# Performance work log

Hardware: AMD Instinct MI355X
Metric: run time of the kernel (lower is better)

## Reference

```python
import jax, jax.numpy as jnp
import numpy as np

B, S, D = 2, 2048, 1024
H, HD = 16, 64


def setup_inputs() -> dict:
    key = jax.random.key(0)
    ks = jax.random.split(key, 6)
    hidden_states = jax.random.normal(ks[0], (B, S, D), dtype=jnp.float32)
    c_attn_w = jax.random.normal(ks[1], (D, 3 * D), dtype=jnp.float32) * 0.02
    c_attn_b = jnp.zeros((3 * D,), dtype=jnp.float32)
    c_proj_w = jax.random.normal(ks[2], (D, D), dtype=jnp.float32) * 0.02
    c_proj_b = jnp.zeros((D,), dtype=jnp.float32)
    basis = jax.random.normal(ks[3], (H, HD, HD), dtype=jnp.float32) * 0.1
    projectors = jnp.einsum('hdr,her->hde', basis, basis)  # basis @ basis.T per head
    return {
        'hidden_states': hidden_states,
        'c_attn_w': c_attn_w,
        'c_attn_b': c_attn_b,
        'c_proj_w': c_proj_w,
        'c_proj_b': c_proj_b,
        'projectors': projectors,
    }


def reference(hidden_states, c_attn_w, c_attn_b, c_proj_w, c_proj_b, projectors):
    # GPT2 Conv1D: out = x @ W + b
    qkv = hidden_states @ c_attn_w + c_attn_b  # [B,S,3D]
    q, k, v = jnp.split(qkv, 3, axis=-1)
    # split heads -> [B,H,S,HD]
    def split_heads(t):
        return t.reshape(B, S, H, HD).transpose(0, 2, 1, 3)
    q, k, v = split_heads(q), split_heads(k), split_heads(v)
    scores = jnp.einsum('bhqd,bhkd->bhqk', q, k) / jnp.sqrt(jnp.float32(HD))
    causal = jnp.tril(jnp.ones((S, S), dtype=bool))
    scores = jnp.where(causal, scores, jnp.finfo(scores.dtype).min)
    probs = jax.nn.softmax(scores, axis=-1)
    attn = jnp.einsum('bhqk,bhkd->bhqd', probs, v)  # [B,H,S,HD]
    # per-head basis projector applied to attention output
    attn = jnp.einsum('bhsd,hde->bhse', attn, projectors)
    # merge heads -> [B,S,D]
    attn = attn.transpose(0, 2, 1, 3).reshape(B, S, D)
    out = attn @ c_proj_w + c_proj_b
    return out
```

## Files before the change

kernel.cpp:

```cpp
#include <hip/hip_runtime.h>
#include <hip/hip_bf16.h>

typedef __attribute__((ext_vector_type(8))) short bhalf8;
typedef __attribute__((ext_vector_type(4))) float f32x4;
typedef __attribute__((ext_vector_type(8))) unsigned short u16x8;
typedef __attribute__((ext_vector_type(4))) unsigned short u16x4;

#define BDIM 2
#define SDIM 2048
#define DDIM 1024
#define HDIM 16
#define HDHD 64
#define EXPB 12.0f

#define GLD16(gaddr, laddr)                                                          \
  __builtin_amdgcn_global_load_lds(                                                  \
      (const __attribute__((address_space(1))) unsigned int*)(gaddr),                \
      (__attribute__((address_space(3))) unsigned int*)(laddr), 16, 0, 0)

__device__ __forceinline__ unsigned short f2bf(float f) {
  unsigned u = __builtin_bit_cast(unsigned, f);
  u += 0x7fffu + ((u >> 16) & 1u);
  return (unsigned short)(u >> 16);
}
__device__ __forceinline__ unsigned short f2bfc(float f) {
  return __builtin_bit_cast(unsigned short, __float2bfloat16(f));
}
__device__ __forceinline__ float bf2f(unsigned short u) {
  return __builtin_bit_cast(float, (unsigned)u << 16);
}

__global__ __launch_bounds__(256) void cvt_hidden(const float* __restrict__ x,
                                                  unsigned short* __restrict__ y) {
  size_t i = ((size_t)blockIdx.x * 256 + threadIdx.x) * 4;
  f32x4 v = *(const f32x4*)(x + i);
  u16x4 o;
  o[0] = f2bf(v[0]); o[1] = f2bf(v[1]); o[2] = f2bf(v[2]); o[3] = f2bf(v[3]);
  *(u16x4*)(y + i) = o;
}

__global__ __launch_bounds__(256) void transpose_cvt(const float* __restrict__ W,
                                                     unsigned short* __restrict__ Wt,
                                                     int R, int C) {
  __shared__ float tl[32][33];
  int rt = blockIdx.x * 32, ct = blockIdx.y * 32;
  int r8 = threadIdx.x >> 5, c = threadIdx.x & 31;
#pragma unroll
  for (int i = 0; i < 4; i++)
    tl[r8 + i * 8][c] = W[(size_t)(rt + r8 + i * 8) * C + ct + c];
  __syncthreads();
#pragma unroll
  for (int i = 0; i < 4; i++)
    Wt[(size_t)(ct + r8 + i * 8) * R + rt + c] = f2bf(tl[c][r8 + i * 8]);
}

__global__ __launch_bounds__(256) void make_wproj(const float* __restrict__ proj,
                                                  const float* __restrict__ wproj,
                                                  unsigned short* __restrict__ WT) {
  int h = blockIdx.x, ot = blockIdx.y * 64;
  __shared__ float Pl[64][65];
  __shared__ float Wl[64][65];
  int t = threadIdx.x;
#pragma unroll
  for (int i = 0; i < 16; i++) {
    int idx = t + 256 * i;
    int a = idx >> 6, bc = idx & 63;
    Pl[a][bc] = proj[(size_t)h * 4096 + idx];
    Wl[a][bc] = wproj[(size_t)(h * 64 + a) * 1024 + ot + bc];
  }
  __syncthreads();
  int d = t & 63, ob = t >> 6;
#pragma unroll
  for (int i = 0; i < 16; i++) {
    int o = ob + i * 4;
    float acc = 0.f;
#pragma unroll
    for (int e = 0; e < 64; e++) acc += Pl[d][e] * Wl[e][o];
    WT[(size_t)(ot + o) * 1024 + h * 64 + d] = f2bf(acc);
  }
}

__global__ __launch_bounds__(256) void gemm_qkv(
    const unsigned short* __restrict__ A, const unsigned short* __restrict__ Bt,
    const float* __restrict__ bias,
    unsigned short* __restrict__ q, unsigned short* __restrict__ k,
    unsigned short* __restrict__ v, int M, int N, int K) {
  __shared__ unsigned short As[128 * 64];
  __shared__ unsigned short Bs[128 * 64];
  const int tid = threadIdx.x;
  const int orig = blockIdx.y * 24 + blockIdx.x;
  const int swz = (orig & 7) * 96 + (orig >> 3);
  const int m0 = (swz / 24) * 128, n0 = (swz % 24) * 128;
  f32x4 acc[4][4];
#pragma unroll
  for (int m = 0; m < 4; m++)
#pragma unroll
    for (int n = 0; n < 4; n++) acc[m][n] = f32x4{0.f, 0.f, 0.f, 0.f};
  const int w = tid >> 6, lane = tid & 63;
  const int wr = (w >> 1) * 64, wc = (w & 1) * 64;
  const int lrow = lane & 15, lg = lane >> 4;

  for (int kt = 0; kt < K; kt += 64) {
    __syncthreads();
#pragma unroll
    for (int i = 0; i < 4; i++) {
      int cl = tid + 256 * i;
      int r = cl >> 3, c = cl & 7;
      int sc = (c ^ (r & 7)) * 8;
      GLD16(A + (size_t)(m0 + r) * K + kt + sc, &As[cl * 8]);
      GLD16(Bt + (size_t)(n0 + r) * K + kt + sc, &Bs[cl * 8]);
    }
    __syncthreads();
#pragma unroll
    for (int kk = 0; kk < 2; kk++) {
      bhalf8 af[4], bfr[4];
#pragma unroll
      for (int m = 0; m < 4; m++) {
        int r = wr + m * 16 + lrow;
        int ch = r * 8 + ((kk * 4 + lg) ^ (r & 7));
        af[m] = *(const bhalf8*)(&As[ch * 8]);
      }
#pragma unroll
      for (int n = 0; n < 4; n++) {
        int r = wc + n * 16 + lrow;
        int ch = r * 8 + ((kk * 4 + lg) ^ (r & 7));
        bfr[n] = *(const bhalf8*)(&Bs[ch * 8]);
      }
#pragma unroll
      for (int m = 0; m < 4; m++)
#pragma unroll
        for (int n = 0; n < 4; n++)
          acc[m][n] = __builtin_amdgcn_mfma_f32_16x16x32_bf16(af[m], bfr[n], acc[m][n], 0, 0, 0);
    }
  }
  const int g = lane >> 4, il = lane & 15;
#pragma unroll
  for (int m = 0; m < 4; m++) {
    int rowb = wr + m * 16 + 4 * g;
#pragma unroll
    for (int n = 0; n < 4; n++) {
      int col = n0 + wc + n * 16 + il;
      float bs = bias[col];
#pragma unroll
      for (int r = 0; r < 4; r++) {
        int row = m0 + rowb + r;
        float val = acc[m][n][r] + bs;
        int which = col >> 10, hh = (col >> 6) & 15, hd = col & 63;
        int b = row >> 11, s = row & 2047;
        size_t idx = ((size_t)(b * 16 + hh) * SDIM + s) * HDHD + hd;
        unsigned short bv = f2bf(which == 0 ? val * 0.1803368801f : val);
        if (which == 0) q[idx] = bv;
        else if (which == 1) k[idx] = bv;
        else v[idx] = bv;
      }
    }
  }
}

__global__ __launch_bounds__(128) void gemm_out(
    const unsigned short* __restrict__ A, const unsigned short* __restrict__ Bt,
    const float* __restrict__ bias, float* __restrict__ Cf, int M, int N, int K) {
  __shared__ unsigned short As[64][72];
  __shared__ unsigned short Bs[128][72];
  const int tid = threadIdx.x;
  const int orig = blockIdx.y * 8 + blockIdx.x;
  const int swz = (orig & 7) * 64 + (orig >> 3);
  const int m0 = (swz / 8) * 64, n0 = (swz % 8) * 128;
  f32x4 acc[4][4];
#pragma unroll
  for (int m = 0; m < 4; m++)
#pragma unroll
    for (int n = 0; n < 4; n++) acc[m][n] = f32x4{0.f, 0.f, 0.f, 0.f};
  const int w = tid >> 6, lane = tid & 63;
  const int wc = w * 64;
  const int lrow = lane & 15, lk = (lane >> 4) * 8;

  for (int kt = 0; kt < K; kt += 64) {
    __syncthreads();
#pragma unroll
    for (int i = 0; i < 4; i++) {
      int cch = tid + 128 * i;
      int r = cch >> 3, c8 = cch & 7;
      *(u16x8*)(&As[r][c8 * 8]) = *(const u16x8*)(A + (size_t)(m0 + r) * K + kt + c8 * 8);
    }
#pragma unroll
    for (int i = 0; i < 8; i++) {
      int cch = tid + 128 * i;
      int r = cch >> 3, c8 = cch & 7;
      *(u16x8*)(&Bs[r][c8 * 8]) = *(const u16x8*)(Bt + (size_t)(n0 + r) * K + kt + c8 * 8);
    }
    __syncthreads();
#pragma unroll
    for (int kk = 0; kk < 2; kk++) {
      bhalf8 af[4], bfr[4];
#pragma unroll
      for (int m = 0; m < 4; m++) af[m] = *(const bhalf8*)(&As[m * 16 + lrow][kk * 32 + lk]);
#pragma unroll
      for (int n = 0; n < 4; n++) bfr[n] = *(const bhalf8*)(&Bs[wc + n * 16 + lrow][kk * 32 + lk]);
#pragma unroll
      for (int m = 0; m < 4; m++)
#pragma unroll
        for (int n = 0; n < 4; n++)
          acc[m][n] = __builtin_amdgcn_mfma_f32_16x16x32_bf16(af[m], bfr[n], acc[m][n], 0, 0, 0);
    }
  }
  const int g = lane >> 4, il = lane & 15;
#pragma unroll
  for (int m = 0; m < 4; m++) {
    int rowb = m * 16 + 4 * g;
#pragma unroll
    for (int n = 0; n < 4; n++) {
      int col = n0 + wc + n * 16 + il;
      float bs = bias[col];
#pragma unroll
      for (int r = 0; r < 4; r++)
        Cf[(size_t)(m0 + rowb + r) * N + col] = acc[m][n][r] + bs;
    }
  }
}

__global__ __launch_bounds__(128, 3) void attn_partial(const unsigned short* __restrict__ Q,
                                                       const unsigned short* __restrict__ Kb,
                                                       const unsigned short* __restrict__ Vb,
                                                       unsigned short* __restrict__ PO,
                                                       float2* __restrict__ ML) {
  __shared__ unsigned short Ks[64][72];
  __shared__ unsigned short Vt[64][72];
  __shared__ unsigned short Ps[2][32][72];
  const int bh = blockIdx.x;
  const int qt = 31 - blockIdx.y;
  const int seg = blockIdx.z;
  const int a = qt >> 3, bq = qt & 7;
  const int nseg = a + 1;
  if (seg >= nseg) return;
  const int k0 = seg * 8;
  const int k1 = min(k0 + 8, qt + 1);

  const int tid = threadIdx.x;
  const int w = tid >> 6, lane = tid & 63;
  const int g = lane >> 4, il = lane & 15;
  const int qbase = qt * 64 + w * 32;
  const size_t bhS = (size_t)bh * SDIM;

  bhalf8 qf[2][2];
#pragma unroll
  for (int f = 0; f < 2; f++) {
    const unsigned short* qp = Q + (bhS + qbase + f * 16 + il) * HDHD + g * 8;
    qf[f][0] = *(const bhalf8*)(qp);
    qf[f][1] = *(const bhalf8*)(qp + 32);
  }
  f32x4 oacc[2][4];
#pragma unroll
  for (int f = 0; f < 2; f++)
#pragma unroll
    for (int i = 0; i < 4; i++) oacc[f][i] = f32x4{0.f, 0.f, 0.f, 0.f};
  float lrun[2] = {0.f, 0.f};

  const int krow = tid >> 1;
  const int kchk = (tid & 1) * 32;
  const int vd0 = (tid & 31) * 2;
  const int vkg = (tid >> 5) * 16;

  u16x8 kr[4];
  unsigned vr[16];
  {
    const size_t kb0 = (bhS + (size_t)k0 * 64) * HDHD;
    const unsigned short* ksrc = Kb + kb0 + krow * HDHD + kchk;
#pragma unroll
    for (int i = 0; i < 4; i++) kr[i] = *(const u16x8*)(ksrc + i * 8);
    const unsigned short* vsrc = Vb + kb0 + (size_t)vkg * HDHD + vd0;
#pragma unroll
    for (int i = 0; i < 16; i++) vr[i] = *(const unsigned*)(vsrc + i * HDHD);
  }

  for (int kt = k0; kt < k1; kt++) {
    __syncthreads();
#pragma unroll
    for (int i = 0; i < 4; i++) *(u16x8*)(&Ks[krow][kchk + i * 8]) = kr[i];
    {
      u16x8 lo0, lo1, hi0, hi1;
#pragma unroll
      for (int i = 0; i < 8; i++) {
        lo0[i] = (unsigned short)(vr[i] & 0xffffu); hi0[i] = (unsigned short)(vr[i] >> 16);
      }
#pragma unroll
      for (int i = 0; i < 8; i++) {
        lo1[i] = (unsigned short)(vr[8 + i] & 0xffffu); hi1[i] = (unsigned short)(vr[8 + i] >> 16);
      }
      *(u16x8*)(&Vt[vd0][vkg]) = lo0;     *(u16x8*)(&Vt[vd0][vkg + 8]) = lo1;
      *(u16x8*)(&Vt[vd0 + 1][vkg]) = hi0; *(u16x8*)(&Vt[vd0 + 1][vkg + 8]) = hi1;
    }
    if (kt + 1 < k1) {
      const size_t kbn = (bhS + (size_t)(kt + 1) * 64) * HDHD;
      const unsigned short* ksrc = Kb + kbn + krow * HDHD + kchk;
#pragma unroll
      for (int i = 0; i < 4; i++) kr[i] = *(const u16x8*)(ksrc + i * 8);
      const unsigned short* vsrc = Vb + kbn + (size_t)vkg * HDHD + vd0;
#pragma unroll
      for (int i = 0; i < 16; i++) vr[i] = *(const unsigned*)(vsrc + i * HDHD);
    }
    __syncthreads();
    f32x4 s[2][4];
#pragma unroll
    for (int f = 0; f < 2; f++)
#pragma unroll
      for (int c = 0; c < 4; c++) s[f][c] = f32x4{0.f, 0.f, 0.f, 0.f};
#pragma unroll
    for (int c = 0; c < 4; c++) {
      bhalf8 kf0 = *(const bhalf8*)(&Ks[c * 16 + il][g * 8]);
      bhalf8 kf1 = *(const bhalf8*)(&Ks[c * 16 + il][32 + g * 8]);
#pragma unroll
      for (int f = 0; f < 2; f++) {
        s[f][c] = __builtin_amdgcn_mfma_f32_16x16x32_bf16(kf0, qf[f][0], s[f][c], 0, 0, 0);
        s[f][c] = __builtin_amdgcn_mfma_f32_16x16x32_bf16(kf1, qf[f][1], s[f][c], 0, 0, 0);
      }
    }
    const bool diag = (kt == qt);
#pragma unroll
    for (int f = 0; f < 2; f++) {
      const int thr = w * 32 + f * 16 + il;
      float rs = 0.f;
#pragma unroll
      for (int c = 0; c < 4; c++) {
        u16x4 pk;
#pragma unroll
        for (int r = 0; r < 4; r++) {
          float v = s[f][c][r];
          if (diag && (c * 16 + 4 * g + r > thr)) v = -1e30f;
          float pv = exp2f(v - EXPB);
          rs += pv;
          pk[r] = f2bfc(pv);
        }
        *(u16x4*)(&Ps[w][f * 16 + il][c * 16 + 4 * g]) = pk;
      }
      rs += __shfl_xor(rs, 16);
      rs += __shfl_xor(rs, 32);
      lrun[f] += rs;
    }
#pragma unroll
    for (int kk = 0; kk < 2; kk++) {
      bhalf8 pf0 = *(const bhalf8*)(&Ps[w][il][kk * 32 + g * 8]);
      bhalf8 pf1 = *(const bhalf8*)(&Ps[w][16 + il][kk * 32 + g * 8]);
#pragma unroll
      for (int df = 0; df < 4; df++) {
        bhalf8 vf = *(const bhalf8*)(&Vt[df * 16 + il][kk * 32 + g * 8]);
        oacc[0][df] = __builtin_amdgcn_mfma_f32_16x16x32_bf16(vf, pf0, oacc[0][df], 0, 0, 0);
        oacc[1][df] = __builtin_amdgcn_mfma_f32_16x16x32_bf16(vf, pf1, oacc[1][df], 0, 0, 0);
      }
    }
  }
  const int pidx = bh * 80 + 4 * a * (a + 1) + bq * (a + 1) + seg;
  __syncthreads();
#pragma unroll
  for (int f = 0; f < 2; f++) {
    float inv = 1.f / lrun[f];
#pragma unroll
    for (int df = 0; df < 4; df++) {
      u16x4 o;
#pragma unroll
      for (int r = 0; r < 4; r++) o[r] = f2bfc(oacc[f][df][r] * inv);
      *(u16x4*)(&Ks[w * 32 + f * 16 + il][df * 16 + 4 * g]) = o;
    }
  }
  if (g == 0) {
#pragma unroll
    for (int f = 0; f < 2; f++)
      ML[(size_t)pidx * 64 + w * 32 + f * 16 + il] = make_float2(EXPB, lrun[f]);
  }
  __syncthreads();
  {
    const int row = tid >> 1, half = (tid & 1) * 32;
    unsigned short* dst = PO + (size_t)pidx * 4096 + (size_t)row * 64 + half;
#pragma unroll
    for (int c8 = 0; c8 < 4; c8++)
      *(u16x8*)(dst + c8 * 8) = *(const u16x8*)(&Ks[row][half + c8 * 8]);
  }
}

__global__ __launch_bounds__(256) void attn_reduce(const unsigned short* __restrict__ PO,
                                                   const float2* __restrict__ ML,
                                                   unsigned short* __restrict__ Om) {
  const int bh = blockIdx.x, qt = blockIdx.y;
  const int a = qt >> 3, bq = qt & 7;
  const int nseg = a + 1;
  const int base = bh * 80 + 4 * a * (a + 1) + bq * (a + 1);
  const int t = threadIdx.x;
  const int r = t >> 2, dc = (t & 3) * 16;
  float2 mls[4];
  float M = -1e30f;
#pragma unroll
  for (int s = 0; s < 4; s++) {
    if (s < nseg) { mls[s] = ML[(size_t)(base + s) * 64 + r]; M = fmaxf(M, mls[s].x); }
  }
  float L = 0.f;
  float O[16];
#pragma unroll
  for (int j = 0; j < 16; j++) O[j] = 0.f;
#pragma unroll
  for (int s = 0; s < 4; s++) {
    if (s < nseg) {
      float wgt = mls[s].y * exp2f(mls[s].x - M);
      L += wgt;
      const unsigned short* p = PO + (size_t)(base + s) * 4096 + r * 64 + dc;
      u16x8 p0 = *(const u16x8*)p, p1 = *(const u16x8*)(p + 8);
#pragma unroll
      for (int j = 0; j < 8; j++) O[j] += wgt * bf2f(p0[j]);
#pragma unroll
      for (int j = 0; j < 8; j++) O[8 + j] += wgt * bf2f(p1[j]);
    }
  }
  float inv = 1.f / L;
  const int b = bh >> 4, h = bh & 15;
  size_t orow = ((size_t)b * SDIM + qt * 64 + r) * DDIM + h * HDHD + dc;
  u16x8 o0, o1;
#pragma unroll
  for (int j = 0; j < 8; j++) o0[j] = f2bfc(O[j] * inv);
#pragma unroll
  for (int j = 0; j < 8; j++) o1[j] = f2bfc(O[8 + j] * inv);
  *(u16x8*)(Om + orow) = o0;
  *(u16x8*)(Om + orow + 8) = o1;
}

__global__ __launch_bounds__(128, 2) void attn_direct(const unsigned short* __restrict__ Q,
                                                      const unsigned short* __restrict__ Kb,
                                                      const unsigned short* __restrict__ Vb,
                                                      unsigned short* __restrict__ Om) {
  __shared__ unsigned short Ks[64][72];
  __shared__ unsigned short Vt[64][72];
  __shared__ unsigned short Ps[2][32][72];
  const int bh = blockIdx.x;
  const int qt = 31 - blockIdx.y;
  const int tid = threadIdx.x;
  const int w = tid >> 6, lane = tid & 63;
  const int g = lane >> 4, il = lane & 15;
  const int qbase = qt * 64 + w * 32;
  const size_t bhS = (size_t)bh * SDIM;
  bhalf8 qf[2][2];
#pragma unroll
  for (int f = 0; f < 2; f++) {
    const unsigned short* qp = Q + (bhS + qbase + f * 16 + il) * HDHD + g * 8;
    qf[f][0] = *(const bhalf8*)(qp);
    qf[f][1] = *(const bhalf8*)(qp + 32);
  }
  f32x4 oacc[2][4];
#pragma unroll
  for (int f = 0; f < 2; f++)
#pragma unroll
    for (int i = 0; i < 4; i++) oacc[f][i] = f32x4{0.f, 0.f, 0.f, 0.f};
  float lrun[2] = {0.f, 0.f};
  const int krow = tid >> 1, kchk = (tid & 1) * 32;
  const int vd0 = (tid & 31) * 2, vkg = (tid >> 5) * 16;
  const int nt = qt + 1;
  for (int kt = 0; kt < nt; kt++) {
    const size_t kbase = (bhS + (size_t)kt * 64) * HDHD;
    __syncthreads();
    {
      const unsigned short* src = Kb + kbase + krow * HDHD + kchk;
#pragma unroll
      for (int i = 0; i < 4; i++) *(u16x8*)(&Ks[krow][kchk + i * 8]) = *(const u16x8*)(src + i * 8);
    }
    {
      const unsigned short* vsrc = Vb + kbase + (size_t)vkg * HDHD + vd0;
      u16x8 lo0, lo1, hi0, hi1;
#pragma unroll
      for (int i = 0; i < 8; i++) {
        unsigned vv = *(const unsigned*)(vsrc + i * HDHD);
        lo0[i] = (unsigned short)(vv & 0xffffu); hi0[i] = (unsigned short)(vv >> 16);
      }
#pragma unroll
      for (int i = 0; i < 8; i++) {
        unsigned vv = *(const unsigned*)(vsrc + (8 + i) * HDHD);
        lo1[i] = (unsigned short)(vv & 0xffffu); hi1[i] = (unsigned short)(vv >> 16);
      }
      *(u16x8*)(&Vt[vd0][vkg]) = lo0;     *(u16x8*)(&Vt[vd0][vkg + 8]) = lo1;
      *(u16x8*)(&Vt[vd0 + 1][vkg]) = hi0; *(u16x8*)(&Vt[vd0 + 1][vkg + 8]) = hi1;
    }
    __syncthreads();
    f32x4 s[2][4];
#pragma unroll
    for (int f = 0; f < 2; f++)
#pragma unroll
      for (int c = 0; c < 4; c++) s[f][c] = f32x4{0.f, 0.f, 0.f, 0.f};
#pragma unroll
    for (int c = 0; c < 4; c++) {
      bhalf8 kf0 = *(const bhalf8*)(&Ks[c * 16 + il][g * 8]);
      bhalf8 kf1 = *(const bhalf8*)(&Ks[c * 16 + il][32 + g * 8]);
#pragma unroll
      for (int f = 0; f < 2; f++) {
        s[f][c] = __builtin_amdgcn_mfma_f32_16x16x32_bf16(kf0, qf[f][0], s[f][c], 0, 0, 0);
        s[f][c] = __builtin_amdgcn_mfma_f32_16x16x32_bf16(kf1, qf[f][1], s[f][c], 0, 0, 0);
      }
    }
    const bool diag = (kt == qt);
#pragma unroll
    for (int f = 0; f < 2; f++) {
      const int thr = w * 32 + f * 16 + il;
      float rs = 0.f;
#pragma unroll
      for (int c = 0; c < 4; c++) {
        u16x4 pk;
#pragma unroll
        for (int r = 0; r < 4; r++) {
          float v = s[f][c][r];
          if (diag && (c * 16 + 4 * g + r > thr)) v = -1e30f;
          float pv = exp2f(v - EXPB);
          rs += pv;
          pk[r] = f2bfc(pv);
        }
        *(u16x4*)(&Ps[w][f * 16 + il][c * 16 + 4 * g]) = pk;
      }
      rs += __shfl_xor(rs, 16);
      rs += __shfl_xor(rs, 32);
      lrun[f] += rs;
    }
#pragma unroll
    for (int kk = 0; kk < 2; kk++) {
      bhalf8 pf0 = *(const bhalf8*)(&Ps[w][il][kk * 32 + g * 8]);
      bhalf8 pf1 = *(const bhalf8*)(&Ps[w][16 + il][kk * 32 + g * 8]);
#pragma unroll
      for (int df = 0; df < 4; df++) {
        bhalf8 vf = *(const bhalf8*)(&Vt[df * 16 + il][kk * 32 + g * 8]);
        oacc[0][df] = __builtin_amdgcn_mfma_f32_16x16x32_bf16(vf, pf0, oacc[0][df], 0, 0, 0);
        oacc[1][df] = __builtin_amdgcn_mfma_f32_16x16x32_bf16(vf, pf1, oacc[1][df], 0, 0, 0);
      }
    }
  }
  __syncthreads();
#pragma unroll
  for (int f = 0; f < 2; f++) {
    float inv = 1.f / lrun[f];
#pragma unroll
    for (int df = 0; df < 4; df++) {
      u16x4 o;
#pragma unroll
      for (int r = 0; r < 4; r++) o[r] = f2bfc(oacc[f][df][r] * inv);
      *(u16x4*)(&Ks[w * 32 + f * 16 + il][df * 16 + 4 * g]) = o;
    }
  }
  __syncthreads();
  {
    const int row = tid >> 1, half = (tid & 1) * 32;
    const int b = bh >> 4, h = bh & 15;
    size_t obase = ((size_t)b * SDIM + qt * 64 + row) * DDIM + h * HDHD + half;
#pragma unroll
    for (int c8 = 0; c8 < 4; c8++)
      *(u16x8*)(Om + obase + c8 * 8) = *(const u16x8*)(&Ks[row][half + c8 * 8]);
  }
}

extern "C" void kernel_launch(void* const* d_in, const int* in_sizes, int n_in,
                              void* d_out, int out_size, void* d_ws, size_t ws_size,
                              hipStream_t stream) {
  const float* hidden = (const float*)d_in[0];
  const float* attn_w = (const float*)d_in[1];
  const float* attn_b = (const float*)d_in[2];
  const float* proj_w = (const float*)d_in[3];
  const float* proj_b = (const float*)d_in[4];
  const float* projectors = (const float*)d_in[5];
  float* out = (float*)d_out;
  char* ws = (char*)d_ws;
  (void)in_sizes; (void)n_in; (void)out_size;

  unsigned short* hseq   = (unsigned short*)(ws);
  unsigned short* wqkvT  = (unsigned short*)(ws + 8388608);
  unsigned short* qb     = (unsigned short*)(ws + 14680064);
  unsigned short* kb     = (unsigned short*)(ws + 23068672);
  unsigned short* vb     = (unsigned short*)(ws + 31457280);
  unsigned short* attnM  = (unsigned short*)(ws + 39845888);
  unsigned short* wprojT = (unsigned short*)(ws + 48234496);
  unsigned short* PO     = (unsigned short*)(ws + 50331648);
  float2*         ML2    = (float2*)(ws + 71303168);
  const size_t ws_needed = 71303168 + 1310720;

  cvt_hidden<<<dim3(4096), dim3(256), 0, stream>>>(hidden, hseq);
  transpose_cvt<<<dim3(32, 96), dim3(256), 0, stream>>>(attn_w, wqkvT, 1024, 3072);
  make_wproj<<<dim3(16, 16), dim3(256), 0, stream>>>(projectors, proj_w, wprojT);
  gemm_qkv<<<dim3(24, 32), dim3(256), 0, stream>>>(hseq, wqkvT, attn_b,
                                                   qb, kb, vb, 4096, 3072, 1024);
  if (ws_size >= ws_needed) {
    attn_partial<<<dim3(32, 32, 4), dim3(128), 0, stream>>>(qb, kb, vb, PO, ML2);
    attn_reduce<<<dim3(32, 32), dim3(256), 0, stream>>>(PO, ML2, attnM);
  } else {
    attn_direct<<<dim3(32, 32), dim3(128), 0, stream>>>(qb, kb, vb, attnM);
  }
  gemm_out<<<dim3(8, 64), dim3(128), 0, stream>>>(attnM, wprojT, proj_b, out,
                                                  4096, 1024, 1024);
}
```

Measured before the change: 162.3 us.

## Process two key tiles per attention iteration and fuse preprocessing kernels

```diff
diff --git a/kernel.cpp b/kernel.cpp
--- a/kernel.cpp
+++ b/kernel.cpp
@@ -30,53 +30,56 @@
   return __builtin_bit_cast(float, (unsigned)u << 16);
 }
 
-__global__ __launch_bounds__(256) void cvt_hidden(const float* __restrict__ x,
-                                                  unsigned short* __restrict__ y) {
-  size_t i = ((size_t)blockIdx.x * 256 + threadIdx.x) * 4;
-  f32x4 v = *(const f32x4*)(x + i);
-  u16x4 o;
-  o[0] = f2bf(v[0]); o[1] = f2bf(v[1]); o[2] = f2bf(v[2]); o[3] = f2bf(v[3]);
-  *(u16x4*)(y + i) = o;
-}
-
-__global__ __launch_bounds__(256) void transpose_cvt(const float* __restrict__ W,
-                                                     unsigned short* __restrict__ Wt,
-                                                     int R, int C) {
-  __shared__ float tl[32][33];
-  int rt = blockIdx.x * 32, ct = blockIdx.y * 32;
-  int r8 = threadIdx.x >> 5, c = threadIdx.x & 31;
-#pragma unroll
-  for (int i = 0; i < 4; i++)
-    tl[r8 + i * 8][c] = W[(size_t)(rt + r8 + i * 8) * C + ct + c];
-  __syncthreads();
-#pragma unroll
-  for (int i = 0; i < 4; i++)
-    Wt[(size_t)(ct + r8 + i * 8) * R + rt + c] = f2bf(tl[c][r8 + i * 8]);
-}
-
-__global__ __launch_bounds__(256) void make_wproj(const float* __restrict__ proj,
+__global__ __launch_bounds__(256) void preprocess(const float* __restrict__ hidden,
+                                                  unsigned short* __restrict__ hseq,
+                                                  const float* __restrict__ attn_w,
+                                                  unsigned short* __restrict__ wqkvT,
+                                                  const float* __restrict__ proj,
                                                   const float* __restrict__ wproj,
-                                                  unsigned short* __restrict__ WT) {
-  int h = blockIdx.x, ot = blockIdx.y * 64;
-  __shared__ float Pl[64][65];
-  __shared__ float Wl[64][65];
-  int t = threadIdx.x;
-#pragma unroll
-  for (int i = 0; i < 16; i++) {
-    int idx = t + 256 * i;
-    int a = idx >> 6, bc = idx & 63;
-    Pl[a][bc] = proj[(size_t)h * 4096 + idx];
-    Wl[a][bc] = wproj[(size_t)(h * 64 + a) * 1024 + ot + bc];
-  }
-  __syncthreads();
-  int d = t & 63, ob = t >> 6;
-#pragma unroll
-  for (int i = 0; i < 16; i++) {
-    int o = ob + i * 4;
-    float acc = 0.f;
-#pragma unroll
-    for (int e = 0; e < 64; e++) acc += Pl[d][e] * Wl[e][o];
-    WT[(size_t)(ot + o) * 1024 + h * 64 + d] = f2bf(acc);
+                                                  unsigned short* __restrict__ wprojT) {
+  __shared__ float smem[2 * 64 * 65];
+  const int bid = blockIdx.x;
+  const int t = threadIdx.x;
+  if (bid < 4096) {
+    size_t i = ((size_t)bid * 256 + t) * 4;
+    f32x4 v = *(const f32x4*)(hidden + i);
+    u16x4 o;
+    o[0] = f2bf(v[0]); o[1] = f2bf(v[1]); o[2] = f2bf(v[2]); o[3] = f2bf(v[3]);
+    *(u16x4*)(hseq + i) = o;
+  } else if (bid < 7168) {
+    float (*tl)[33] = (float(*)[33])smem;
+    const int tt = bid - 4096;
+    const int rt = (tt & 31) * 32, ct = (tt >> 5) * 32;
+    const int r8 = t >> 5, c = t & 31;
+#pragma unroll
+    for (int i = 0; i < 4; i++)
+      tl[r8 + i * 8][c] = attn_w[(size_t)(rt + r8 + i * 8) * 3072 + ct + c];
+    __syncthreads();
+#pragma unroll
+    for (int i = 0; i < 4; i++)
+      wqkvT[(size_t)(ct + r8 + i * 8) * 1024 + rt + c] = f2bf(tl[c][r8 + i * 8]);
+  } else {
+    float (*Pl)[65] = (float(*)[65])smem;
+    float (*Wl)[65] = (float(*)[65])(smem + 64 * 65);
+    const int tt = bid - 7168;
+    const int h = tt & 15, ot = (tt >> 4) * 64;
+#pragma unroll
+    for (int i = 0; i < 16; i++) {
+      int idx = t + 256 * i;
+      int a = idx >> 6, bc = idx & 63;
+      Pl[a][bc] = proj[(size_t)h * 4096 + idx];
+      Wl[a][bc] = wproj[(size_t)(h * 64 + a) * 1024 + ot + bc];
+    }
+    __syncthreads();
+    int d = t & 63, ob = t >> 6;
+#pragma unroll
+    for (int i = 0; i < 16; i++) {
+      int o = ob + i * 4;
+      float acc = 0.f;
+#pragma unroll
+      for (int e = 0; e < 64; e++) acc += Pl[d][e] * Wl[e][o];
+      wprojT[(size_t)(ot + o) * 1024 + h * 64 + d] = f2bf(acc);
+    }
   }
 }
 
@@ -219,14 +222,14 @@
   }
 }
 
-__global__ __launch_bounds__(128, 3) void attn_partial(const unsigned short* __restrict__ Q,
+__global__ __launch_bounds__(128, 2) void attn_partial(const unsigned short* __restrict__ Q,
                                                        const unsigned short* __restrict__ Kb,
                                                        const unsigned short* __restrict__ Vb,
                                                        unsigned short* __restrict__ PO,
                                                        float2* __restrict__ ML) {
-  __shared__ unsigned short Ks[64][72];
-  __shared__ unsigned short Vt[64][72];
-  __shared__ unsigned short Ps[2][32][72];
+  __shared__ unsigned short Ks[128][72];
+  __shared__ unsigned short Vt[64][136];
+  __shared__ unsigned short Ps[2][32][136];
   const int bh = blockIdx.x;
   const int qt = 31 - blockIdx.y;
   const int seg = blockIdx.z;
@@ -256,89 +259,96 @@
     for (int i = 0; i < 4; i++) oacc[f][i] = f32x4{0.f, 0.f, 0.f, 0.f};
   float lrun[2] = {0.f, 0.f};
 
-  const int krow = tid >> 1;
-  const int kchk = (tid & 1) * 32;
   const int vd0 = (tid & 31) * 2;
   const int vkg = (tid >> 5) * 16;
 
-  u16x8 kr[4];
-  unsigned vr[16];
-  {
-    const size_t kb0 = (bhS + (size_t)k0 * 64) * HDHD;
-    const unsigned short* ksrc = Kb + kb0 + krow * HDHD + kchk;
-#pragma unroll
-    for (int i = 0; i < 4; i++) kr[i] = *(const u16x8*)(ksrc + i * 8);
-    const unsigned short* vsrc = Vb + kb0 + (size_t)vkg * HDHD + vd0;
-#pragma unroll
-    for (int i = 0; i < 16; i++) vr[i] = *(const unsigned*)(vsrc + i * HDHD);
-  }
-
-  for (int kt = k0; kt < k1; kt++) {
-    __syncthreads();
-#pragma unroll
-    for (int i = 0; i < 4; i++) *(u16x8*)(&Ks[krow][kchk + i * 8]) = kr[i];
-    {
+  u16x8 kr[8];
+  unsigned vr[32];
+#define LOADP(ktv)                                                                    \
+  {                                                                                   \
+    const unsigned short* ksrc = Kb + (bhS + (size_t)(ktv) * 64 + tid) * HDHD;        \
+    _Pragma("unroll")                                                                 \
+    for (int i = 0; i < 8; i++) kr[i] = *(const u16x8*)(ksrc + i * 8);                \
+    _Pragma("unroll")                                                                 \
+    for (int h = 0; h < 2; h++) {                                                     \
+      const unsigned short* vsrc =                                                    \
+          Vb + (bhS + (size_t)((ktv) + h) * 64 + vkg) * HDHD + vd0;                   \
+      _Pragma("unroll")                                                               \
+      for (int i = 0; i < 16; i++) vr[h * 16 + i] = *(const unsigned*)(vsrc + i * HDHD); \
+    }                                                                                 \
+  }
+
+  LOADP(k0);
+
+  for (int kt = k0; kt < k1; kt += 2) {
+    __syncthreads();
+#pragma unroll
+    for (int i = 0; i < 8; i++) *(u16x8*)(&Ks[tid][i * 8]) = kr[i];
+#pragma unroll
+    for (int h = 0; h < 2; h++) {
       u16x8 lo0, lo1, hi0, hi1;
 #pragma unroll
       for (int i = 0; i < 8; i++) {
-        lo0[i] = (unsigned short)(vr[i] & 0xffffu); hi0[i] = (unsigned short)(vr[i] >> 16);
+        unsigned vv = vr[h * 16 + i];
+        lo0[i] = (unsigned short)(vv & 0xffffu); hi0[i] = (unsigned short)(vv >> 16);
       }
 #pragma unroll
       for (int i = 0; i < 8; i++) {
-        lo1[i] = (unsigned short)(vr[8 + i] & 0xffffu); hi1[i] = (unsigned short)(vr[8 + i] >> 16);
-      }
-      *(u16x8*)(&Vt[vd0][vkg]) = lo0;     *(u16x8*)(&Vt[vd0][vkg + 8]) = lo1;
-      *(u16x8*)(&Vt[vd0 + 1][vkg]) = hi0; *(u16x8*)(&Vt[vd0 + 1][vkg + 8]) = hi1;
-    }
-    if (kt + 1 < k1) {
-      const size_t kbn = (bhS + (size_t)(kt + 1) * 64) * HDHD;
-      const unsigned short* ksrc = Kb + kbn + krow * HDHD + kchk;
-#pragma unroll
-      for (int i = 0; i < 4; i++) kr[i] = *(const u16x8*)(ksrc + i * 8);
-      const unsigned short* vsrc = Vb + kbn + (size_t)vkg * HDHD + vd0;
-#pragma unroll
-      for (int i = 0; i < 16; i++) vr[i] = *(const unsigned*)(vsrc + i * HDHD);
-    }
-    __syncthreads();
-    f32x4 s[2][4];
-#pragma unroll
-    for (int f = 0; f < 2; f++)
-#pragma unroll
-      for (int c = 0; c < 4; c++) s[f][c] = f32x4{0.f, 0.f, 0.f, 0.f};
-#pragma unroll
-    for (int c = 0; c < 4; c++) {
-      bhalf8 kf0 = *(const bhalf8*)(&Ks[c * 16 + il][g * 8]);
-      bhalf8 kf1 = *(const bhalf8*)(&Ks[c * 16 + il][32 + g * 8]);
+        unsigned vv = vr[h * 16 + 8 + i];
+        lo1[i] = (unsigned short)(vv & 0xffffu); hi1[i] = (unsigned short)(vv >> 16);
+      }
+      *(u16x8*)(&Vt[vd0][h * 64 + vkg]) = lo0;     *(u16x8*)(&Vt[vd0][h * 64 + vkg + 8]) = lo1;
+      *(u16x8*)(&Vt[vd0 + 1][h * 64 + vkg]) = hi0; *(u16x8*)(&Vt[vd0 + 1][h * 64 + vkg + 8]) = hi1;
+    }
+    if (kt + 2 < k1) LOADP(kt + 2);
+    __syncthreads();
+    float rs[2] = {0.f, 0.f};
+#pragma unroll
+    for (int h = 0; h < 2; h++) {
+      f32x4 s[2][4];
+#pragma unroll
+      for (int f = 0; f < 2; f++)
+#pragma unroll
+        for (int c = 0; c < 4; c++) s[f][c] = f32x4{0.f, 0.f, 0.f, 0.f};
+#pragma unroll
+      for (int c = 0; c < 4; c++) {
+        bhalf8 kf0 = *(const bhalf8*)(&Ks[h * 64 + c * 16 + il][g * 8]);
+        bhalf8 kf1 = *(const bhalf8*)(&Ks[h * 64 + c * 16 + il][32 + g * 8]);
+#pragma unroll
+        for (int f = 0; f < 2; f++) {
+          s[f][c] = __builtin_amdgcn_mfma_f32_16x16x32_bf16(kf0, qf[f][0], s[f][c], 0, 0, 0);
+          s[f][c] = __builtin_amdgcn_mfma_f32_16x16x32_bf16(kf1, qf[f][1], s[f][c], 0, 0, 0);
+        }
+      }
+      const int rel = (kt + h - qt) * 64;
 #pragma unroll
       for (int f = 0; f < 2; f++) {
-        s[f][c] = __builtin_amdgcn_mfma_f32_16x16x32_bf16(kf0, qf[f][0], s[f][c], 0, 0, 0);
-        s[f][c] = __builtin_amdgcn_mfma_f32_16x16x32_bf16(kf1, qf[f][1], s[f][c], 0, 0, 0);
-      }
-    }
-    const bool diag = (kt == qt);
+        const int thr = w * 32 + f * 16 + il;
+#pragma unroll
+        for (int c = 0; c < 4; c++) {
+          u16x4 pk;
+#pragma unroll
+          for (int r = 0; r < 4; r++) {
+            float v = s[f][c][r];
+            int ck = c * 16 + 4 * g + r;
+            if (rel + ck > thr) v = -1e30f;
+            float pv = exp2f(v - EXPB);
+            rs[f] += pv;
+            pk[r] = f2bfc(pv);
+          }
+          *(u16x4*)(&Ps[w][f * 16 + il][h * 64 + c * 16 + 4 * g]) = pk;
+        }
+      }
+    }
 #pragma unroll
     for (int f = 0; f < 2; f++) {
-      const int thr = w * 32 + f * 16 + il;
-      float rs = 0.f;
-#pragma unroll
-      for (int c = 0; c < 4; c++) {
-        u16x4 pk;
-#pragma unroll
-        for (int r = 0; r < 4; r++) {
-          float v = s[f][c][r];
-          if (diag && (c * 16 + 4 * g + r > thr)) v = -1e30f;
-          float pv = exp2f(v - EXPB);
-          rs += pv;
-          pk[r] = f2bfc(pv);
-        }
-        *(u16x4*)(&Ps[w][f * 16 + il][c * 16 + 4 * g]) = pk;
-      }
-      rs += __shfl_xor(rs, 16);
-      rs += __shfl_xor(rs, 32);
-      lrun[f] += rs;
-    }
-#pragma unroll
-    for (int kk = 0; kk < 2; kk++) {
+      float t = rs[f];
+      t += __shfl_xor(t, 16);
+      t += __shfl_xor(t, 32);
+      lrun[f] += t;
+    }
+#pragma unroll
+    for (int kk = 0; kk < 4; kk++) {
       bhalf8 pf0 = *(const bhalf8*)(&Ps[w][il][kk * 32 + g * 8]);
       bhalf8 pf1 = *(const bhalf8*)(&Ps[w][16 + il][kk * 32 + g * 8]);
 #pragma unroll
@@ -349,6 +359,7 @@
       }
     }
   }
+#undef LOADP
   const int pidx = bh * 80 + 4 * a * (a + 1) + bq * (a + 1) + seg;
   __syncthreads();
 #pragma unroll
@@ -572,9 +583,8 @@
   float2*         ML2    = (float2*)(ws + 71303168);
   const size_t ws_needed = 71303168 + 1310720;
 
-  cvt_hidden<<<dim3(4096), dim3(256), 0, stream>>>(hidden, hseq);
-  transpose_cvt<<<dim3(32, 96), dim3(256), 0, stream>>>(attn_w, wqkvT, 1024, 3072);
-  make_wproj<<<dim3(16, 16), dim3(256), 0, stream>>>(projectors, proj_w, wprojT);
+  preprocess<<<dim3(7424), dim3(256), 0, stream>>>(hidden, hseq, attn_w, wqkvT,
+                                                   projectors, proj_w, wprojT);
   gemm_qkv<<<dim3(24, 32), dim3(256), 0, stream>>>(hseq, wqkvT, attn_b,
                                                    qb, kb, vb, 4096, 3072, 1024);
   if (ws_size >= ws_needed) {
```

After: 181.2 us. 11.6% more time.
